# Kernel optimization log

Measured on AMD Instinct MI355X. Metric: run time of the kernel, lower is better.

## Reference

```python
import jax, jax.numpy as jnp
import numpy as np
import itertools


def setup_inputs() -> dict:
    key = jax.random.key(0)
    k1, k2 = jax.random.split(key)
    B, D, H, W, C = 2, 160, 160, 160, 2
    vol = jax.random.normal(k1, (B, D, H, W, C), dtype=jnp.float32)
    # dense displacement field, a few voxels of motion (typical registration flow)
    trf = jax.random.normal(k2, (B, D, H, W, 3), dtype=jnp.float32) * 3.0
    return {"vol": vol, "trf": trf}


def _interp_single(vol, shift):
    """vol: [D,H,W,C], shift: [D,H,W,3] -> warped [D,H,W,C].
    Faithful to transform()+interpn(interp_method='linear', indexing='ij')."""
    volshape = vol.shape[:-1]
    nd = len(volshape)  # 3
    # mesh + shift = absolute sample locations (float)
    mesh = jnp.meshgrid(*[jnp.arange(d, dtype=jnp.float32) for d in volshape],
                        indexing='ij')
    loc = jnp.stack(mesh, axis=-1) + shift  # [D,H,W,3]

    loc0 = jnp.floor(loc)
    max_loc = jnp.array([d - 1 for d in volshape], dtype=jnp.float32)  # [3]
    loc0c = jnp.clip(loc0, 0.0, max_loc)          # clipped floor corner
    loc1c = jnp.clip(loc0c + 1.0, 0.0, max_loc)   # clipped ceil corner

    # NOTE: weights use clipped loc1 vs UNclipped loc, exactly as the TF code
    d1 = loc1c - loc        # weight paired with corner bit 0 (floor)
    d0 = 1.0 - d1           # weight paired with corner bit 1 (ceil)
    locs = (loc0c.astype(jnp.int32), loc1c.astype(jnp.int32))
    wts = (d1, d0)

    out = jnp.zeros(volshape + (vol.shape[-1],), dtype=vol.dtype)
    # 2^3 = 8 corner gathers + weighted accumulation (same as sub2ind + tf.gather)
    for c in itertools.product([0, 1], repeat=nd):
        idx = tuple(locs[c[d]][..., d] for d in range(nd))
        w = wts[c[0]][..., 0] * wts[c[1]][..., 1] * wts[c[2]][..., 2]
        out = out + w[..., None] * vol[idx]
    return out


def reference(vol, trf):
    # single_transform=False: per-sample warp (tf.map_fn over batch)
    return jax.vmap(_interp_single)(vol, trf)
```

## Files before the change

kernel.cpp:

```cpp
#include <hip/hip_runtime.h>


#define BLK 256
constexpr int Bn = 2, Dn = 160, Hn = 160, Wn = 160;
constexpr int HQ = 40;
constexpr int RSTRIP = HQ * Wn;
constexpr int V = 4;

typedef float f32x2 __attribute__((ext_vector_type(2)));
typedef float f32x4 __attribute__((ext_vector_type(4), aligned(8)));

__global__ __launch_bounds__(BLK, 4) void st_warp_kernel(
    const float* __restrict__ vol,
    const float* __restrict__ trf,
    float* __restrict__ out)
{
    const int tid = threadIdx.x;
    const int xcd = blockIdx.x & 7;
    const int j   = blockIdx.x >> 3;
    const int b   = xcd >> 2;
    const int h0  = (xcd & 3) * HQ;

    int   gvox[V];
    float sd[V], sh[V], sw[V];
    #pragma unroll
    for (int k = 0; k < V; ++k) {
        const int v   = j * (BLK * V) + k * BLK + tid;
        const int d   = v / RSTRIP;
        const int rem = v - d * RSTRIP;
        const int hh  = rem / Wn;
        const int w   = rem - hh * Wn;
        gvox[k] = ((b * Dn + d) * Hn + (h0 + hh)) * Wn + w;
    }
    #pragma unroll
    for (int k = 0; k < V; ++k) {
        const float* tp = trf + (long long)gvox[k] * 3;
        sd[k] = __builtin_nontemporal_load(tp + 0);
        sh[k] = __builtin_nontemporal_load(tp + 1);
        sw[k] = __builtin_nontemporal_load(tp + 2);
    }

    f32x4 val[4 * V];
    float wA[V], wB[V], wC[V], wD[V], w0[V], w1[V];
    #pragma unroll
    for (int k = 0; k < V; ++k) {
        const int v   = j * (BLK * V) + k * BLK + tid;
        const int d   = v / RSTRIP;
        const int rem = v - d * RSTRIP;
        const int hh  = rem / Wn;
        const int w   = rem - hh * Wn;
        const int h   = h0 + hh;

        float loc, c0f, c1f;

        loc = (float)d + sd[k];
        c0f = fminf(fmaxf(floorf(loc), 0.0f), (float)(Dn - 1));
        c1f = fminf(c0f + 1.0f, (float)(Dn - 1));
        const float wd0 = c1f - loc, wd1 = 1.0f - wd0;
        const int id0 = (int)c0f, id1 = (int)c1f;

        loc = (float)h + sh[k];
        c0f = fminf(fmaxf(floorf(loc), 0.0f), (float)(Hn - 1));
        c1f = fminf(c0f + 1.0f, (float)(Hn - 1));
        const float wh0 = c1f - loc, wh1 = 1.0f - wh0;
        const int ih0 = (int)c0f, ih1 = (int)c1f;

        loc = (float)w + sw[k];
        c0f = fminf(fmaxf(floorf(loc), 0.0f), (float)(Wn - 1));
        c1f = fminf(c0f + 1.0f, (float)(Wn - 1));
        const float ww0 = c1f - loc, ww1 = 1.0f - ww0;
        const int iw0 = (int)c0f;

        const bool lo = (iw0 < Wn - 1);
        const int  m  = lo ? iw0 : (Wn - 2);
        w0[k] = lo ? ww0 : 0.0f;
        w1[k] = lo ? ww1 : 1.0f;
        wA[k] = wd0 * wh0; wB[k] = wd0 * wh1;
        wC[k] = wd1 * wh0; wD[k] = wd1 * wh1;

        const int bo  = b * Dn;
        const int r00 = ((bo + id0) * Hn + ih0) * Wn;
        const int r01 = ((bo + id0) * Hn + ih1) * Wn;
        const int r10 = ((bo + id1) * Hn + ih0) * Wn;
        const int r11 = ((bo + id1) * Hn + ih1) * Wn;

        val[4 * k + 0] = *(const f32x4*)(vol + (((long long)(r00 + m)) << 1));
        val[4 * k + 1] = *(const f32x4*)(vol + (((long long)(r01 + m)) << 1));
        val[4 * k + 2] = *(const f32x4*)(vol + (((long long)(r10 + m)) << 1));
        val[4 * k + 3] = *(const f32x4*)(vol + (((long long)(r11 + m)) << 1));
    }

    #pragma unroll
    for (int k = 0; k < V; ++k) {
        const f32x4 vA = val[4 * k + 0], vB = val[4 * k + 1];
        const f32x4 vC = val[4 * k + 2], vD = val[4 * k + 3];
        const float acc0 = wA[k] * (w0[k] * vA.x + w1[k] * vA.z)
                         + wB[k] * (w0[k] * vB.x + w1[k] * vB.z)
                         + wC[k] * (w0[k] * vC.x + w1[k] * vC.z)
                         + wD[k] * (w0[k] * vD.x + w1[k] * vD.z);
        const float acc1 = wA[k] * (w0[k] * vA.y + w1[k] * vA.w)
                         + wB[k] * (w0[k] * vB.y + w1[k] * vB.w)
                         + wC[k] * (w0[k] * vC.y + w1[k] * vC.w)
                         + wD[k] * (w0[k] * vD.y + w1[k] * vD.w);
        f32x2 res; res.x = acc0; res.y = acc1;
        __builtin_nontemporal_store(res, &((f32x2*)out)[gvox[k]]);
    }
}

extern "C" void kernel_launch(void* const* d_in, const int* in_sizes, int n_in,
                              void* d_out, int out_size, void* d_ws, size_t ws_size,
                              hipStream_t stream) {
    const float* vol = (const float*)d_in[0];
    const float* trf = (const float*)d_in[1];
    float* out = (float*)d_out;

    const int nvox = Bn * Dn * Hn * Wn;
    const int grid = nvox / (BLK * V);
    st_warp_kernel<<<grid, BLK, 0, stream>>>(vol, trf, out);
}
```

Measured before the change: 311.5 us.

## Repack volume into fp16 H-pair layout to halve trilinear gather loads

Adds a pre-pass that converts the fp32 volume to fp16 in a workspace. Each entry packs a voxel, its W neighbor and the matching voxels in the next H row (clamped at the edge). The warp kernel then fetches each voxel's 8 corners with two 16-byte loads instead of four, which reduces scattered gather traffic. In exchange every call pays an extra full read and write of the volume. The fp16 storage also adds rounding error to the sampled values. The fp32 kernel remains as a fallback when the workspace is too small.

```diff
diff --git a/kernel.cpp b/kernel.cpp
--- a/kernel.cpp
+++ b/kernel.cpp
@@ -7,10 +7,128 @@
 constexpr int RSTRIP = HQ * Wn;
 constexpr int V = 4;
 
-typedef float f32x2 __attribute__((ext_vector_type(2)));
-typedef float f32x4 __attribute__((ext_vector_type(4), aligned(8)));
-
-__global__ __launch_bounds__(BLK, 4) void st_warp_kernel(
+typedef float    f32x2 __attribute__((ext_vector_type(2)));
+typedef float    f32x4 __attribute__((ext_vector_type(4), aligned(8)));
+typedef _Float16 h16x8 __attribute__((ext_vector_type(8), aligned(8)));
+
+__global__ __launch_bounds__(BLK) void repack_h_pairs(
+    const float* __restrict__ vol, _Float16* __restrict__ pk)
+{
+    const int t  = blockIdx.x * BLK + threadIdx.x;
+    const int v0 = t * 2;
+    const int w  = v0 % Wn;
+    const int r  = v0 / Wn;
+    const int h  = r % Hn;
+    const int hc = (h < Hn - 1) ? (h + 1) : h;
+    const int r1 = r - h + hc;
+
+    const f32x4 a = *(const f32x4*)(vol + ((long long)v0 << 1));
+    const f32x4 b = *(const f32x4*)(vol + ((long long)(r1 * Wn + w) << 1));
+
+    h16x8 o;
+    o[0] = (_Float16)a.x; o[1] = (_Float16)a.y;
+    o[2] = (_Float16)b.x; o[3] = (_Float16)b.y;
+    o[4] = (_Float16)a.z; o[5] = (_Float16)a.w;
+    o[6] = (_Float16)b.z; o[7] = (_Float16)b.w;
+    *(h16x8*)(pk + ((long long)v0 << 2)) = o;
+}
+
+__global__ __launch_bounds__(BLK, 4) void st_warp_kernel_pk(
+    const _Float16* __restrict__ pk,
+    const float* __restrict__ trf,
+    float* __restrict__ out)
+{
+    const int tid = threadIdx.x;
+    const int xcd = blockIdx.x & 7;
+    const int j   = blockIdx.x >> 3;
+    const int b   = xcd >> 2;
+    const int h0  = (xcd & 3) * HQ;
+
+    int   gvox[V];
+    float sd[V], sh[V], sw[V];
+    #pragma unroll
+    for (int k = 0; k < V; ++k) {
+        const int v   = j * (BLK * V) + k * BLK + tid;
+        const int d   = v / RSTRIP;
+        const int rem = v - d * RSTRIP;
+        const int hh  = rem / Wn;
+        const int w   = rem - hh * Wn;
+        gvox[k] = ((b * Dn + d) * Hn + (h0 + hh)) * Wn + w;
+    }
+    #pragma unroll
+    for (int k = 0; k < V; ++k) {
+        const float* tp = trf + (long long)gvox[k] * 3;
+        sd[k] = __builtin_nontemporal_load(tp + 0);
+        sh[k] = __builtin_nontemporal_load(tp + 1);
+        sw[k] = __builtin_nontemporal_load(tp + 2);
+    }
+
+    h16x8 val[2 * V];
+    float wA[V], wB[V], wC[V], wD[V], w0[V], w1[V];
+    #pragma unroll
+    for (int k = 0; k < V; ++k) {
+        const int v   = j * (BLK * V) + k * BLK + tid;
+        const int d   = v / RSTRIP;
+        const int rem = v - d * RSTRIP;
+        const int hh  = rem / Wn;
+        const int w   = rem - hh * Wn;
+        const int h   = h0 + hh;
+
+        float loc, c0f, c1f;
+
+        loc = (float)d + sd[k];
+        c0f = fminf(fmaxf(floorf(loc), 0.0f), (float)(Dn - 1));
+        c1f = fminf(c0f + 1.0f, (float)(Dn - 1));
+        const float wd0 = c1f - loc, wd1 = 1.0f - wd0;
+        const int id0 = (int)c0f, id1 = (int)c1f;
+
+        loc = (float)h + sh[k];
+        c0f = fminf(fmaxf(floorf(loc), 0.0f), (float)(Hn - 1));
+        c1f = fminf(c0f + 1.0f, (float)(Hn - 1));
+        const float wh0 = c1f - loc, wh1 = 1.0f - wh0;
+        const int ih0 = (int)c0f;
+
+        loc = (float)w + sw[k];
+        c0f = fminf(fmaxf(floorf(loc), 0.0f), (float)(Wn - 1));
+        c1f = fminf(c0f + 1.0f, (float)(Wn - 1));
+        const float ww0 = c1f - loc, ww1 = 1.0f - ww0;
+        const int iw0 = (int)c0f;
+
+        const bool lo = (iw0 < Wn - 1);
+        const int  m  = lo ? iw0 : (Wn - 2);
+        w0[k] = lo ? ww0 : 0.0f;
+        w1[k] = lo ? ww1 : 1.0f;
+        wA[k] = wd0 * wh0; wB[k] = wd0 * wh1;
+        wC[k] = wd1 * wh0; wD[k] = wd1 * wh1;
+
+        const int bo = b * Dn;
+        const int p0 = ((bo + id0) * Hn + ih0) * Wn + m;
+        const int p1 = ((bo + id1) * Hn + ih0) * Wn + m;
+
+        val[2 * k + 0] = *(const h16x8*)(pk + ((long long)p0 << 2));
+        val[2 * k + 1] = *(const h16x8*)(pk + ((long long)p1 << 2));
+    }
+
+    #pragma unroll
+    for (int k = 0; k < V; ++k) {
+        const h16x8 a = val[2 * k + 0];
+        const h16x8 c = val[2 * k + 1];
+        const float acc0 =
+              wA[k] * (w0[k] * (float)a[0] + w1[k] * (float)a[4])
+            + wB[k] * (w0[k] * (float)a[2] + w1[k] * (float)a[6])
+            + wC[k] * (w0[k] * (float)c[0] + w1[k] * (float)c[4])
+            + wD[k] * (w0[k] * (float)c[2] + w1[k] * (float)c[6]);
+        const float acc1 =
+              wA[k] * (w0[k] * (float)a[1] + w1[k] * (float)a[5])
+            + wB[k] * (w0[k] * (float)a[3] + w1[k] * (float)a[7])
+            + wC[k] * (w0[k] * (float)c[1] + w1[k] * (float)c[5])
+            + wD[k] * (w0[k] * (float)c[3] + w1[k] * (float)c[7]);
+        f32x2 res; res.x = acc0; res.y = acc1;
+        __builtin_nontemporal_store(res, &((f32x2*)out)[gvox[k]]);
+    }
+}
+
+__global__ __launch_bounds__(BLK, 4) void st_warp_kernel_f32(
     const float* __restrict__ vol,
     const float* __restrict__ trf,
     float* __restrict__ out)
@@ -116,5 +234,14 @@
 
     const int nvox = Bn * Dn * Hn * Wn;
     const int grid = nvox / (BLK * V);
-    st_warp_kernel<<<grid, BLK, 0, stream>>>(vol, trf, out);
-}
+    const size_t pk_bytes = (size_t)nvox * 4 * sizeof(_Float16);
+
+    if (d_ws != nullptr && ws_size >= pk_bytes) {
+        _Float16* pk = (_Float16*)d_ws;
+        const int rgrid = (nvox / 2) / BLK;
+        repack_h_pairs<<<rgrid, BLK, 0, stream>>>(vol, pk);
+        st_warp_kernel_pk<<<grid, BLK, 0, stream>>>(pk, trf, out);
+    } else {
+        st_warp_kernel_f32<<<grid, BLK, 0, stream>>>(vol, trf, out);
+    }
+}
```

Measured after the change: 278.2 us. -10.7%, faster.
